# Performance work log

Hardware: AMD Instinct MI355X
Metric: run time of the kernel (lower is better)

## Reference

```python
import jax, jax.numpy as jnp
import numpy as np

N, C, G = 200000, 64, 128  # points, channels, grid size
K = 27  # 3^3 kernel offsets


def _build_neighbor_idx(seed=0):
    rng = np.random.default_rng(seed)
    lin = rng.choice(G ** 3, size=N, replace=False).astype(np.int64)
    x = lin // (G * G)
    y = (lin // G) % G
    z = lin % G
    table = np.full(G ** 3, -1, dtype=np.int64)
    table[lin] = np.arange(N, dtype=np.int64)
    nbr = np.full((N, K), -1, dtype=np.int32)
    k = 0
    for dx in (-1, 0, 1):
        for dy in (-1, 0, 1):
            for dz in (-1, 0, 1):
                xn, yn, zn = x + dx, y + dy, z + dz
                valid = ((xn >= 0) & (xn < G) & (yn >= 0) & (yn < G)
                         & (zn >= 0) & (zn < G))
                nl = xn * (G * G) + yn * G + zn
                nbr[valid, k] = table[nl[valid]].astype(np.int32)
                k += 1
    return jnp.asarray(nbr)


def setup_inputs() -> dict:
    key = jax.random.key(0)
    ks = jax.random.split(key, 4)
    scale = 0.05
    return {
        "feats": jax.random.normal(ks[0], (N, C), jnp.float32),
        "W1": jax.random.normal(ks[1], (K, C, C), jnp.float32) * scale,
        "b1": jnp.zeros((C,), jnp.float32),
        "W2": jax.random.normal(ks[2], (K, C, C), jnp.float32) * scale,
        "b2": jnp.zeros((C,), jnp.float32),
        "W3": jax.random.normal(ks[3], (K, C, 2 * C), jnp.float32) * scale,
        "b3": jnp.zeros((2 * C,), jnp.float32),
        "neighbor_idx": _build_neighbor_idx(),
    }


def _sparse_conv(feats, nbr, W, b):
    # out[j] = sum_k feats[nbr[j,k]] @ W[k], skipping missing neighbors (-1).
    n = feats.shape[0]
    out = jnp.zeros((n, W.shape[-1]), feats.dtype)
    idx = jnp.maximum(nbr, 0)
    mask = (nbr >= 0).astype(feats.dtype)
    for k in range(W.shape[0]):  # fixed small loop over 27 kernel offsets
        g = feats[idx[:, k]] * mask[:, k][:, None]  # [N, Cin]
        out = out + g @ W[k]
    return out + b


def reference(feats, W1, b1, W2, b2, W3, b3, neighbor_idx):
    h = jax.nn.relu(_sparse_conv(feats, neighbor_idx, W1, b1))
    h = jax.nn.relu(_sparse_conv(h, neighbor_idx, W2, b2))
    out = _sparse_conv(h, neighbor_idx, W3, b3)  # [N, 2C]
    return out
```

## Files before the change

kernel.cpp:

```cpp
#include <hip/hip_runtime.h>
#include <hip/hip_bf16.h>

#define NPTS 200000
#define CIN 64
#define KOFF 27
#define MTILE 128

typedef __attribute__((ext_vector_type(8))) short bf16x8;
typedef __attribute__((ext_vector_type(4))) float f32x4;

__device__ inline void gload16(const void* g, void* lds) {
  __builtin_amdgcn_global_load_lds(
      (const __attribute__((address_space(1))) void*)g,
      (__attribute__((address_space(3))) void*)lds, 16, 0, 0);
}

__device__ inline ushort f2bf(float f) {
  union { float f; unsigned u; } x; x.f = f;
  unsigned r = (x.u + 0x7fffu + ((x.u >> 16) & 1u)) >> 16;
  return (ushort)r;
}

__global__ void cvt_bf16_kernel(const float* __restrict__ in,
                                ushort* __restrict__ out, int n4) {
  int stride = gridDim.x * blockDim.x;
  for (int i = blockIdx.x * blockDim.x + threadIdx.x; i < n4; i += stride) {
    float4 v = ((const float4*)in)[i];
    ushort4 o;
    o.x = f2bf(v.x); o.y = f2bf(v.y); o.z = f2bf(v.z); o.w = f2bf(v.w);
    ((ushort4*)out)[i] = o;
  }
}

__global__ void cvt_wt_kernel(const float* __restrict__ W,
                              ushort* __restrict__ Wt, int Co) {
  int total = KOFF * CIN * Co;
  for (int i = blockIdx.x * blockDim.x + threadIdx.x; i < total;
       i += gridDim.x * blockDim.x) {
    int k = i / (CIN * Co);
    int rem = i - k * (CIN * Co);
    int co = rem / CIN;
    int c = rem - co * CIN;
    Wt[i] = f2bf(W[k * CIN * Co + c * Co + co]);
  }
}

template <int COUT, bool RELU, bool OUTBF16>
__global__ __launch_bounds__(256, 2)
void layer_kernel(const ushort* __restrict__ inB,
                  const ushort* __restrict__ Wt,
                  const float* __restrict__ bias,
                  const int* __restrict__ nbr,
                  void* __restrict__ outp,
                  const ushort* __restrict__ zpage) {
  __shared__ ushort A_lds[MTILE * CIN];
  __shared__ ushort B_lds[COUT * CIN];
  __shared__ int nbr_lds[MTILE * KOFF];

  const int tid = threadIdx.x;
  const int j0 = blockIdx.x * MTILE;

  for (int idx = tid; idx < MTILE * KOFF; idx += 256) {
    int j = j0 + idx / KOFF;
    nbr_lds[idx] = (j < NPTS) ? nbr[j0 * KOFF + idx] : -1;
  }
  __syncthreads();

  const int w = tid >> 6, l = tid & 63;
  const int llo = l & 15, lhi = l >> 4;

  constexpr int NF = COUT / 16;
  f32x4 acc[2][NF];
  const f32x4 zero4 = {0.f, 0.f, 0.f, 0.f};
#pragma unroll
  for (int m = 0; m < 2; ++m)
#pragma unroll
    for (int n = 0; n < NF; ++n) acc[m][n] = zero4;

  constexpr int AR = (MTILE * CIN * 2) / (256 * 16);
  constexpr int BR = (COUT * CIN * 2) / (256 * 16);

  for (int k = 0; k < KOFF; ++k) {
#pragma unroll
    for (int p = 0; p < AR; ++p) {
      int lin = p * 256 + tid;
      int row = lin >> 3;
      int c = lin & 7;
      int csw = c ^ (row & 7);
      int src = nbr_lds[row * KOFF + k];
      const ushort* g = (src < 0) ? (zpage + csw * 8)
                                  : (inB + src * CIN + csw * 8);
      gload16(g, &A_lds[lin * 8]);
    }
#pragma unroll
    for (int p = 0; p < BR; ++p) {
      int lin = p * 256 + tid;
      int row = lin >> 3;
      int c = lin & 7;
      int csw = c ^ (row & 7);
      gload16(Wt + k * COUT * CIN + row * CIN + csw * 8, &B_lds[lin * 8]);
    }
    __syncthreads();

#pragma unroll
    for (int kk = 0; kk < 2; ++kk) {
      bf16x8 a[2];
#pragma unroll
      for (int m = 0; m < 2; ++m) {
        int row = w * 32 + m * 16 + llo;
        int chunk = (kk * 4 + lhi) ^ (row & 7);
        a[m] = *(const bf16x8*)&A_lds[row * CIN + chunk * 8];
      }
#pragma unroll
      for (int n = 0; n < NF; ++n) {
        int brow = n * 16 + llo;
        int chunk = (kk * 4 + lhi) ^ (brow & 7);
        bf16x8 b = *(const bf16x8*)&B_lds[brow * CIN + chunk * 8];
#pragma unroll
        for (int m = 0; m < 2; ++m)
          acc[m][n] = __builtin_amdgcn_mfma_f32_16x16x32_bf16(a[m], b,
                                                              acc[m][n], 0, 0, 0);
      }
    }
    __syncthreads();
  }

#pragma unroll
  for (int n = 0; n < NF; ++n) {
    int col = n * 16 + llo;
    float bb = bias[col];
#pragma unroll
    for (int m = 0; m < 2; ++m) {
#pragma unroll
      for (int r = 0; r < 4; ++r) {
        int row = j0 + w * 32 + m * 16 + lhi * 4 + r;
        if (row < NPTS) {
          float x = acc[m][n][r] + bb;
          if (RELU) x = fmaxf(x, 0.f);
          if (OUTBF16)
            ((ushort*)outp)[row * COUT + col] = f2bf(x);
          else
            ((float*)outp)[row * COUT + col] = x;
        }
      }
    }
  }
}

extern "C" void kernel_launch(void* const* d_in, const int* in_sizes, int n_in,
                              void* d_out, int out_size, void* d_ws, size_t ws_size,
                              hipStream_t stream) {
  const float* feats = (const float*)d_in[0];
  const float* W1 = (const float*)d_in[1];
  const float* b1 = (const float*)d_in[2];
  const float* W2 = (const float*)d_in[3];
  const float* b2 = (const float*)d_in[4];
  const float* W3 = (const float*)d_in[5];
  const float* b3 = (const float*)d_in[6];
  const int* nbr = (const int*)d_in[7];

  char* ws = (char*)d_ws;
  ushort* featsB = (ushort*)d_out;
  ushort* h1B = (ushort*)((char*)d_out + 76800000);
  ushort* W1t = (ushort*)(ws);
  ushort* W2t = (ushort*)(ws + 262144);
  ushort* W3t = (ushort*)(ws + 524288);
  ushort* zpage = (ushort*)(ws + 1048576);
  ushort* h2B = (ushort*)(ws + 2097152);

  hipMemsetAsync(zpage, 0, 256, stream);

  cvt_bf16_kernel<<<2048, 256, 0, stream>>>(feats, featsB, NPTS * CIN / 4);
  cvt_wt_kernel<<<256, 256, 0, stream>>>(W1, W1t, 64);
  cvt_wt_kernel<<<256, 256, 0, stream>>>(W2, W2t, 64);
  cvt_wt_kernel<<<512, 256, 0, stream>>>(W3, W3t, 128);

  int grid = (NPTS + MTILE - 1) / MTILE;
  layer_kernel<64, true, true><<<grid, 256, 0, stream>>>(featsB, W1t, b1, nbr, h1B, zpage);
  layer_kernel<64, true, true><<<grid, 256, 0, stream>>>(h1B, W2t, b2, nbr, h2B, zpage);
  layer_kernel<128, false, false><<<grid, 256, 0, stream>>>(h2B, W3t, b3, nbr, d_out, zpage);
}
```

Measured before the change: 439.1 us.

## Compact valid neighbor pairs per offset and scatter-accumulate via LDS atomics

Instead of gathering all 27 neighbor rows per point (mostly zeros for a sparse grid), each block counts valid neighbors per kernel offset, builds compacted 16-row fragments of (source, row) pairs, and runs MFMAs only on those fragments. Results are scattered into an LDS float accumulator with atomic adds, and weights are pre-permuted into MFMA fragment order and read directly from global memory. This removes wasted gather bandwidth and MFMA work on missing neighbors. In exchange it adds LDS atomic contention, per-block pair-building overhead with a serial prefix step, and uncached weight loads per fragment.

```diff
diff --git a/kernel.cpp b/kernel.cpp
--- a/kernel.cpp
+++ b/kernel.cpp
@@ -5,6 +5,8 @@
 #define CIN 64
 #define KOFF 27
 #define MTILE 128
+#define MAXPAIR (MTILE * KOFF)
+#define MAXFRAG (MAXPAIR / 16)
 
 typedef __attribute__((ext_vector_type(8))) short bf16x8;
 typedef __attribute__((ext_vector_type(4))) float f32x4;
@@ -32,116 +34,162 @@
   }
 }
 
+template <int Co>
 __global__ void cvt_wt_kernel(const float* __restrict__ W,
-                              ushort* __restrict__ Wt, int Co) {
+                              ushort* __restrict__ Wt) {
+  constexpr int NF = Co / 16;
   int total = KOFF * CIN * Co;
   for (int i = blockIdx.x * blockDim.x + threadIdx.x; i < total;
        i += gridDim.x * blockDim.x) {
     int k = i / (CIN * Co);
     int rem = i - k * (CIN * Co);
-    int co = rem / CIN;
-    int c = rem - co * CIN;
-    Wt[i] = f2bf(W[k * CIN * Co + c * Co + co]);
-  }
-}
-
-template <int COUT, bool RELU, bool OUTBF16>
-__global__ __launch_bounds__(256, 2)
+    int c = rem / Co;
+    int co = rem - c * Co;
+    int n = co >> 4, llo = co & 15;
+    int kk = c >> 5, lhi = (c >> 3) & 3, e = c & 7;
+    int dest = (((k * NF + n) * 2 + kk) * 64 + lhi * 16 + llo) * 8 + e;
+    Wt[dest] = f2bf(W[i]);
+  }
+}
+
+template <int COUT, bool RELU, bool OUTBF16, int MINW>
+__global__ __launch_bounds__(256, MINW)
 void layer_kernel(const ushort* __restrict__ inB,
                   const ushort* __restrict__ Wt,
                   const float* __restrict__ bias,
                   const int* __restrict__ nbr,
                   void* __restrict__ outp,
                   const ushort* __restrict__ zpage) {
-  __shared__ ushort A_lds[MTILE * CIN];
-  __shared__ ushort B_lds[COUT * CIN];
-  __shared__ int nbr_lds[MTILE * KOFF];
+  constexpr int NF = COUT / 16;
+  constexpr int STRIDE = COUT + 4;
+  __shared__ float acc[MTILE * STRIDE];
+  __shared__ int pairs[MAXPAIR];
+  __shared__ int frag_k[MAXFRAG];
+  __shared__ int cnt[KOFF], offs[KOFF], cur[KOFF];
+  __shared__ int nfrag_s, npad_s;
+  __shared__ ushort A_buf[4][2][16 * CIN];
 
   const int tid = threadIdx.x;
   const int j0 = blockIdx.x * MTILE;
-
-  for (int idx = tid; idx < MTILE * KOFF; idx += 256) {
-    int j = j0 + idx / KOFF;
-    nbr_lds[idx] = (j < NPTS) ? nbr[j0 * KOFF + idx] : -1;
-  }
-  __syncthreads();
-
   const int w = tid >> 6, l = tid & 63;
   const int llo = l & 15, lhi = l >> 4;
 
-  constexpr int NF = COUT / 16;
-  f32x4 acc[2][NF];
-  const f32x4 zero4 = {0.f, 0.f, 0.f, 0.f};
+  for (int i = tid; i < MTILE * STRIDE; i += 256) acc[i] = 0.f;
+  if (tid < KOFF) cnt[tid] = 0;
+  __syncthreads();
+
+  for (int idx = tid; idx < MTILE * KOFF; idx += 256) {
+    int row = idx / KOFF;
+    if (j0 + row < NPTS) {
+      int v = nbr[j0 * KOFF + idx];
+      if (v >= 0) atomicAdd(&cnt[idx - row * KOFF], 1);
+    }
+  }
+  __syncthreads();
+
+  if (tid == 0) {
+    int pos = 0, nf = 0;
+    for (int k = 0; k < KOFF; ++k) {
+      offs[k] = pos; cur[k] = pos;
+      int nfk = (cnt[k] + 15) >> 4;
+      for (int f = 0; f < nfk; ++f) frag_k[nf++] = k;
+      pos += nfk << 4;
+    }
+    nfrag_s = nf; npad_s = pos;
+  }
+  __syncthreads();
+  const int npad = npad_s;
+  for (int i = tid; i < npad; i += 256) pairs[i] = -1;
+  __syncthreads();
+
+  for (int idx = tid; idx < MTILE * KOFF; idx += 256) {
+    int row = idx / KOFF;
+    if (j0 + row < NPTS) {
+      int v = nbr[j0 * KOFF + idx];
+      if (v >= 0) {
+        int k = idx - row * KOFF;
+        int p = atomicAdd(&cur[k], 1);
+        pairs[p] = v * MTILE + row;
+      }
+    }
+  }
+  __syncthreads();
+  const int nfrag = nfrag_s;
+
+  ushort* buf0 = &A_buf[w][0][0];
+  ushort* buf1 = &A_buf[w][1][0];
+
+  auto stage = [&](int f, ushort* buf) {
 #pragma unroll
-  for (int m = 0; m < 2; ++m)
+    for (int i = 0; i < 2; ++i) {
+      int r = i * 8 + (l >> 3);
+      int c = l & 7;
+      int csw = c ^ (r & 7);
+      int pr = pairs[f * 16 + r];
+      const ushort* g = (pr < 0) ? (zpage + csw * 8)
+                                 : (inB + (pr >> 7) * CIN + csw * 8);
+      gload16(g, buf + i * 512 + l * 8);
+    }
+  };
+
+  int myf = w;
+  if (myf < nfrag) stage(myf, buf0);
+  int bufsel = 0;
+  while (myf < nfrag) {
+    int nxt = myf + 4;
+    if (nxt < nfrag) {
+      stage(nxt, bufsel ? buf0 : buf1);
+      asm volatile("s_waitcnt vmcnt(2)" ::: "memory");
+    } else {
+      asm volatile("s_waitcnt vmcnt(0)" ::: "memory");
+    }
+    __builtin_amdgcn_sched_barrier(0);
+
+    const ushort* bufc = bufsel ? buf1 : buf0;
+    bf16x8 a0 = *(const bf16x8*)&bufc[llo * CIN + ((lhi ^ (llo & 7)) * 8)];
+    bf16x8 a1 = *(const bf16x8*)&bufc[llo * CIN + (((4 + lhi) ^ (llo & 7)) * 8)];
+
+    int k = frag_k[myf];
+    const ushort* Wk = Wt + k * (NF * 2 * 64 * 8);
+    int4 pr4 = *(const int4*)&pairs[myf * 16 + lhi * 4];
+    int r0 = pr4.x & (MTILE - 1), r1 = pr4.y & (MTILE - 1);
+    int r2 = pr4.z & (MTILE - 1), r3 = pr4.w & (MTILE - 1);
+
 #pragma unroll
-    for (int n = 0; n < NF; ++n) acc[m][n] = zero4;
-
-  constexpr int AR = (MTILE * CIN * 2) / (256 * 16);
-  constexpr int BR = (COUT * CIN * 2) / (256 * 16);
-
-  for (int k = 0; k < KOFF; ++k) {
-#pragma unroll
-    for (int p = 0; p < AR; ++p) {
-      int lin = p * 256 + tid;
-      int row = lin >> 3;
-      int c = lin & 7;
-      int csw = c ^ (row & 7);
-      int src = nbr_lds[row * KOFF + k];
-      const ushort* g = (src < 0) ? (zpage + csw * 8)
-                                  : (inB + src * CIN + csw * 8);
-      gload16(g, &A_lds[lin * 8]);
-    }
-#pragma unroll
-    for (int p = 0; p < BR; ++p) {
-      int lin = p * 256 + tid;
-      int row = lin >> 3;
-      int c = lin & 7;
-      int csw = c ^ (row & 7);
-      gload16(Wt + k * COUT * CIN + row * CIN + csw * 8, &B_lds[lin * 8]);
-    }
-    __syncthreads();
-
-#pragma unroll
-    for (int kk = 0; kk < 2; ++kk) {
-      bf16x8 a[2];
-#pragma unroll
-      for (int m = 0; m < 2; ++m) {
-        int row = w * 32 + m * 16 + llo;
-        int chunk = (kk * 4 + lhi) ^ (row & 7);
-        a[m] = *(const bf16x8*)&A_lds[row * CIN + chunk * 8];
+    for (int n = 0; n < NF; ++n) {
+      bf16x8 b0 = *(const bf16x8*)&Wk[((n * 2 + 0) * 64 + l) * 8];
+      bf16x8 b1 = *(const bf16x8*)&Wk[((n * 2 + 1) * 64 + l) * 8];
+      f32x4 accf = {0.f, 0.f, 0.f, 0.f};
+      accf = __builtin_amdgcn_mfma_f32_16x16x32_bf16(a0, b0, accf, 0, 0, 0);
+      accf = __builtin_amdgcn_mfma_f32_16x16x32_bf16(a1, b1, accf, 0, 0, 0);
+      int col = n * 16 + llo;
+      atomicAdd(&acc[r0 * STRIDE + col], accf[0]);
+      atomicAdd(&acc[r1 * STRIDE + col], accf[1]);
+      atomicAdd(&acc[r2 * STRIDE + col], accf[2]);
+      atomicAdd(&acc[r3 * STRIDE + col], accf[3]);
+    }
+    myf = nxt; bufsel ^= 1;
+  }
+  __syncthreads();
+
+  for (int i = tid; i < MTILE * COUT / 4; i += 256) {
+    int row = i / (COUT / 4);
+    int c4 = (i - row * (COUT / 4)) * 4;
+    int j = j0 + row;
+    if (j < NPTS) {
+      float4 v = *(const float4*)&acc[row * STRIDE + c4];
+      float4 bb = *(const float4*)&bias[c4];
+      v.x += bb.x; v.y += bb.y; v.z += bb.z; v.w += bb.w;
+      if (RELU) {
+        v.x = fmaxf(v.x, 0.f); v.y = fmaxf(v.y, 0.f);
+        v.z = fmaxf(v.z, 0.f); v.w = fmaxf(v.w, 0.f);
       }
-#pragma unroll
-      for (int n = 0; n < NF; ++n) {
-        int brow = n * 16 + llo;
-        int chunk = (kk * 4 + lhi) ^ (brow & 7);
-        bf16x8 b = *(const bf16x8*)&B_lds[brow * CIN + chunk * 8];
-#pragma unroll
-        for (int m = 0; m < 2; ++m)
-          acc[m][n] = __builtin_amdgcn_mfma_f32_16x16x32_bf16(a[m], b,
-                                                              acc[m][n], 0, 0, 0);
-      }
-    }
-    __syncthreads();
-  }
-
-#pragma unroll
-  for (int n = 0; n < NF; ++n) {
-    int col = n * 16 + llo;
-    float bb = bias[col];
-#pragma unroll
-    for (int m = 0; m < 2; ++m) {
-#pragma unroll
-      for (int r = 0; r < 4; ++r) {
-        int row = j0 + w * 32 + m * 16 + lhi * 4 + r;
-        if (row < NPTS) {
-          float x = acc[m][n][r] + bb;
-          if (RELU) x = fmaxf(x, 0.f);
-          if (OUTBF16)
-            ((ushort*)outp)[row * COUT + col] = f2bf(x);
-          else
-            ((float*)outp)[row * COUT + col] = x;
-        }
+      if (OUTBF16) {
+        ushort4 o; o.x = f2bf(v.x); o.y = f2bf(v.y);
+        o.z = f2bf(v.z); o.w = f2bf(v.w);
+        *(ushort4*)&((ushort*)outp)[j * COUT + c4] = o;
+      } else {
+        *(float4*)&((float*)outp)[j * COUT + c4] = v;
       }
     }
   }
@@ -171,12 +219,12 @@
   hipMemsetAsync(zpage, 0, 256, stream);
 
   cvt_bf16_kernel<<<2048, 256, 0, stream>>>(feats, featsB, NPTS * CIN / 4);
-  cvt_wt_kernel<<<256, 256, 0, stream>>>(W1, W1t, 64);
-  cvt_wt_kernel<<<256, 256, 0, stream>>>(W2, W2t, 64);
-  cvt_wt_kernel<<<512, 256, 0, stream>>>(W3, W3t, 128);
+  cvt_wt_kernel<64><<<256, 256, 0, stream>>>(W1, W1t);
+  cvt_wt_kernel<64><<<256, 256, 0, stream>>>(W2, W2t);
+  cvt_wt_kernel<128><<<512, 256, 0, stream>>>(W3, W3t);
 
   int grid = (NPTS + MTILE - 1) / MTILE;
-  layer_kernel<64, true, true><<<grid, 256, 0, stream>>>(featsB, W1t, b1, nbr, h1B, zpage);
-  layer_kernel<64, true, true><<<grid, 256, 0, stream>>>(h1B, W2t, b2, nbr, h2B, zpage);
-  layer_kernel<128, false, false><<<grid, 256, 0, stream>>>(h2B, W3t, b3, nbr, d_out, zpage);
-}
+  layer_kernel<64, true, true, 2><<<grid, 256, 0, stream>>>(featsB, W1t, b1, nbr, h1B, zpage);
+  layer_kernel<64, true, true, 2><<<grid, 256, 0, stream>>>(h1B, W2t, b2, nbr, h2B, zpage);
+  layer_kernel<128, false, false, 1><<<grid, 256, 0, stream>>>(h2B, W3t, b3, nbr, d_out, zpage);
+}
```

Result: slower. 1.715 ms (+290.6%).
